# Optimization experiments

Measured on AMD Instinct MI355X. Metric: run time of the kernel, lower is better.

## Reference

```python
import jax, jax.numpy as jnp
from jax import lax
import numpy as np

MSS = 1448.0
MAX_RTT = 0.01
B, S = 2048, 4096


def setup_inputs() -> dict:
    key = jax.random.key(0)
    k1, k2, k3, k4 = jax.random.split(key, 4)
    # packet lengths in [0, 1500) bytes so bursts aggregate past MSS=1448
    x = jax.random.uniform(k1, (B, S), jnp.float32) * 1500.0
    mask = jax.random.uniform(k2, (B, S)) < 0.1
    scale = 0.00094557476340694
    d_exp = 1e-6 + scale * jax.random.exponential(k3, (B, S), jnp.float32)
    delays = jnp.where(mask, jnp.float32(0.21), d_exp)
    # per-burst RTT samples, indexed by the burst-start packet position
    rtts = jax.random.uniform(k4, (B, S), jnp.float32) * MAX_RTT
    return {"x": x, "delays": delays, "rtts": rtts}


def _simulate_row(x, delays, rtts):
    # x, delays, rtts: [S]
    S_ = x.shape[0]

    def step(carry, inp):
        active, new_burst, r = carry
        xj, dj, rj = inp
        # outer-while check only at burst start: stop forever if x[j] <= 0
        active = jnp.where(new_burst, active & (xj > 0), active)
        r = jnp.where(new_burst, rj, r)
        r_next = r - dj  # inner while: RTT -= delays[j]
        burst_end = active & (r_next <= 0)
        start_flag = new_burst & active
        return (active, burst_end, r_next), (active, start_flag)

    init = (jnp.bool_(True), jnp.bool_(True), jnp.float32(0.0))
    _, (consumed, start_flag) = lax.scan(step, init, (x, delays, rtts))

    # per-burst buffered byte count: segment-sum of consumed packet lengths
    burst_id = jnp.clip(jnp.cumsum(start_flag.astype(jnp.int32)) - 1, 0, S_ - 1)
    buf = jax.ops.segment_sum(jnp.where(consumed, x, 0.0), burst_id, num_segments=S_)

    # `while buf > MSS` emits ceil(buf/MSS)-1 full segments, then remainder
    n_full = jnp.maximum(jnp.ceil(buf / MSS).astype(jnp.int32) - 1, 0)
    rem = buf - n_full.astype(x.dtype) * MSS
    has_rem = rem > 0
    count = n_full + has_rem.astype(jnp.int32)
    starts = jnp.cumsum(count) - count  # exclusive cumsum: output offset per burst
    ends = starts + n_full

    # difference-array trick: positions in [starts, ends) get MSS (OOB drops == truncation)
    diff = (jnp.zeros(S_, jnp.int32)
            .at[starts].add(1, mode='drop')
            .at[ends].add(-1, mode='drop'))
    cover = jnp.cumsum(diff) > 0
    out = jnp.where(cover, jnp.float32(MSS), jnp.float32(0.0))

    # remainder goes right after the MSS run of its burst
    rem_pos = jnp.where(has_rem, ends, S_)  # S_ -> dropped
    out = out.at[rem_pos].set(rem, mode='drop')
    return out


def reference(x, delays, rtts):
    out = jax.vmap(_simulate_row)(x, delays, rtts)  # [B, S]
    return out[..., None]  # unsqueeze(-1) -> [B, S, 1]
```

## Files before the change

### kernel.cpp

```cpp
#include <hip/hip_runtime.h>
#include <math.h>


#define S_LEN 4096
#define BLOCK 512
#define PER   8
#define MSSF  1448.0f

#define OFF_A    0
#define OFF_JB   8208
#define OFF_NXT  16416
#define OFF_MENT 24624
#define OFF_WS   25648
#define SMEM_SZ  25680

__global__ __launch_bounds__(BLOCK, 8) void traffic_kernel(
    const float* __restrict__ gx,
    const float* __restrict__ gd,
    const float* __restrict__ gr,
    float* __restrict__ gout)
{
    __shared__ __align__(16) unsigned char smem[SMEM_SZ];
    float*          s_dly  = (float*)(smem + OFF_A);
    unsigned short* s_jA   = (unsigned short*)(smem + OFF_A);
    unsigned short* s_jB   = (unsigned short*)(smem + OFF_JB);
    int*            s_diff = (int*)(smem + OFF_A);
    float*          s_out  = (float*)(smem + OFF_A);
    unsigned short* s_nxt  = (unsigned short*)(smem + OFF_NXT);
    unsigned short* s_ment = (unsigned short*)(smem + OFF_MENT);
    int*            s_ws   = (int*)(smem + OFF_WS);

    const int tid = threadIdx.x;
    const int sb  = tid << 3;
    const size_t rowoff = (size_t)blockIdx.x * S_LEN;
    const float* px = gx + rowoff;
    const float* pd = gd + rowoff;
    const float* pr = gr + rowoff;

    float xreg[PER];
    {
        float4 xa = *(const float4*)(px + sb);
        float4 xb = *(const float4*)(px + sb + 4);
        xreg[0]=xa.x; xreg[1]=xa.y; xreg[2]=xa.z; xreg[3]=xa.w;
        xreg[4]=xb.x; xreg[5]=xb.y; xreg[6]=xb.z; xreg[7]=xb.w;
    }
    {
        const float4* pd4 = (const float4*)pd;
        float4* s4 = (float4*)s_dly;
        for (int q = tid; q < S_LEN / 4; q += BLOCK) s4[q] = pd4[q];
        if (tid < 8) s_dly[S_LEN + tid] = 1.0e30f;
    }
    float rt[PER];
#pragma unroll
    for (int i = 0; i < PER; ++i) rt[i] = pr[tid + (i << 9)];
    __syncthreads();

    unsigned surv = 0;
    float rsv[PER];
#pragma unroll
    for (int i = 0; i < PER; ++i) {
        const int p0 = tid + (i << 9);
        const float* dw = s_dly + p0;
        float d0 = dw[0], d1 = dw[1], d2 = dw[2], d3 = dw[3];
        float d4 = dw[4], d5 = dw[5], d6 = dw[6], d7 = dw[7];
        float r1 = rt[i] - d0;
        float r2 = r1 - d1;
        float r3 = r2 - d2;
        float r4 = r3 - d3;
        float r5 = r4 - d4;
        float r6 = r5 - d5;
        float r7 = r6 - d6;
        float r8 = r7 - d7;
        int c = (r1 > 0.0f) + (r2 > 0.0f) + (r3 > 0.0f) + (r4 > 0.0f) +
                (r5 > 0.0f) + (r6 > 0.0f) + (r7 > 0.0f) + (r8 > 0.0f);
        rsv[i] = r8;
        if (c == 8) {
            surv |= 1u << i;
        } else {
            int nx = p0 + c + 1;
            if (nx > S_LEN) nx = S_LEN;
            s_nxt[p0] = (unsigned short)nx;
        }
    }

    while (surv) {
        int i = __ffs(surv) - 1;
        surv &= surv - 1;
        float rr = rsv[0];
#pragma unroll
        for (int ii = 1; ii < PER; ++ii) rr = (i == ii) ? rsv[ii] : rr;
        int p0 = tid + (i << 9);
        int j = p0 + 8;
        int nx;
        while (true) {
            float e0 = s_dly[j],     e1 = s_dly[j + 1];
            float e2 = s_dly[j + 2], e3 = s_dly[j + 3];
            float e4 = s_dly[j + 4], e5 = s_dly[j + 5];
            float e6 = s_dly[j + 6], e7 = s_dly[j + 7];
            float q1 = rr - e0;
            float q2 = q1 - e1;
            float q3 = q2 - e2;
            float q4 = q3 - e3;
            float q5 = q4 - e4;
            float q6 = q5 - e5;
            float q7 = q6 - e6;
            float q8 = q7 - e7;
            int c2 = (q1 > 0.0f) + (q2 > 0.0f) + (q3 > 0.0f) + (q4 > 0.0f) +
                     (q5 > 0.0f) + (q6 > 0.0f) + (q7 > 0.0f) + (q8 > 0.0f);
            if (c2 < 8) { nx = j + c2 + 1; break; }
            j += 8;
            rr = q8;
        }
        if (nx > S_LEN) nx = S_LEN;
        s_nxt[p0] = (unsigned short)nx;
    }
    __syncthreads();

    int nx8[PER];
    unsigned long long rel = 0x8ull << 32;
    {
        uint4 ld = *(const uint4*)&s_nxt[sb];
        nx8[0] = ld.x & 0xFFFF; nx8[1] = ld.x >> 16;
        nx8[2] = ld.y & 0xFFFF; nx8[3] = ld.y >> 16;
        nx8[4] = ld.z & 0xFFFF; nx8[5] = ld.z >> 16;
        nx8[6] = ld.w & 0xFFFF; nx8[7] = ld.w >> 16;
#pragma unroll
        for (int i = 0; i < PER; ++i)
            if (!(xreg[i] > 0.0f)) nx8[i] = S_LEN;
        int ee[PER];
#pragma unroll
        for (int i = PER - 1; i >= 0; --i) {
            int v = nx8[i];
            int e = v;
#pragma unroll
            for (int j2 = i + 1; j2 < PER; ++j2)
                if (v == sb + j2) e = ee[j2];
            ee[i] = e;
        }
        uint4 pk;
        pk.x = (unsigned)ee[0] | ((unsigned)ee[1] << 16);
        pk.y = (unsigned)ee[2] | ((unsigned)ee[3] << 16);
        pk.z = (unsigned)ee[4] | ((unsigned)ee[5] << 16);
        pk.w = (unsigned)ee[6] | ((unsigned)ee[7] << 16);
        *(uint4*)&s_jA[sb] = pk;
#pragma unroll
        for (int i = 0; i < PER; ++i) {
            int r = nx8[i] - sb; if (r > 8) r = 8;
            rel |= (unsigned long long)r << (i << 2);
        }
    }
    if (tid == 0) { s_jA[4096] = (unsigned short)4096; s_jB[4096] = (unsigned short)4096; }
    s_ment[tid] = (tid == 0) ? (unsigned short)1 : (unsigned short)0;
    __syncthreads();

    {
        unsigned short* ja = s_jA;
        unsigned short* jb = s_jB;
        int own[PER];
#pragma unroll
        for (int i = 0; i < PER; ++i) own[i] = (int)ja[tid + (i << 9)];
        for (int k = 0; k < 9; ++k) {
            int ent = (int)s_ment[tid];
            int q = -1;
            if (ent) {
                int e = (int)ja[ent - 1];
                if (e < S_LEN) q = e;
            }
            if (k < 8) {
                int nv[PER];
#pragma unroll
                for (int i = 0; i < PER; ++i) nv[i] = (int)ja[own[i]];
                if (q >= 0) s_ment[q >> 3] = (unsigned short)(q + 1);
#pragma unroll
                for (int i = 0; i < PER; ++i) jb[tid + (i << 9)] = (unsigned short)nv[i];
#pragma unroll
                for (int i = 0; i < PER; ++i) own[i] = nv[i];
            } else {
                if (q >= 0) s_ment[q >> 3] = (unsigned short)(q + 1);
            }
            __syncthreads();
            unsigned short* t = ja; ja = jb; jb = t;
        }
    }

    unsigned lm = 0;
    {
        int ent = (int)s_ment[tid];
        if (ent) {
            int p = ent - 1 - sb;
#pragma unroll
            for (int s = 0; s < PER; ++s) {
                lm |= (p < 8) ? (1u << p) : 0u;
                p = (int)((rel >> (p << 2)) & 15ull);
            }
        }
    }

    float bsum[PER];
    unsigned use = 0;
    int tsum = 0;
#pragma unroll
    for (int i = 0; i < PER; ++i) {
        float buf = 0.0f;
        int c = 0;
        if ((lm >> i) & 1u) {
            float xp = xreg[i];
            if (xp > 0.0f) {
                use |= 1u << i;
                int e = nx8[i];
                int upper = e - sb;
                float sum = xp;
#pragma unroll
                for (int jj = i + 1; jj < PER; ++jj)
                    sum += (jj < upper) ? xreg[jj] : 0.0f;
                for (int j = sb + PER; j < e; ++j) sum += px[j];
                buf = sum;
                int nf = (int)ceilf(buf / MSSF) - 1; if (nf < 0) nf = 0;
                float rem = buf - (float)nf * MSSF;
                c = nf + (rem > 0.0f ? 1 : 0);
            }
        }
        bsum[i] = buf;
        tsum += c;
    }

    {
        int4* d4 = (int4*)s_diff;
        int4 z; z.x = z.y = z.z = z.w = 0;
        d4[tid] = z;
        d4[tid + 512] = z;
    }
    int texcl;
    {
        int lane = tid & 63, wv = tid >> 6;
        int v = tsum;
        for (int off = 1; off < 64; off <<= 1) {
            int u = __shfl_up(v, off, 64);
            if (lane >= off) v += u;
        }
        if (lane == 63) s_ws[wv] = v;
        __syncthreads();
        int woff = 0;
        for (int w = 0; w < wv; ++w) woff += s_ws[w];
        texcl = woff + v - tsum;
    }

    {
        int o = texcl;
#pragma unroll
        for (int i = 0; i < PER; ++i) {
            if ((use >> i) & 1u) {
                float buf = bsum[i];
                int nf = (int)ceilf(buf / MSSF) - 1; if (nf < 0) nf = 0;
                float rem = buf - (float)nf * MSSF;
                if (nf > 0) {
                    if (o < S_LEN) atomicAdd(&s_diff[o], 1);
                    int e2 = o + nf;
                    if (e2 < S_LEN) atomicAdd(&s_diff[e2], -1);
                }
                o += nf + (rem > 0.0f ? 1 : 0);
            }
        }
    }
    __syncthreads();

    {
        int4 a = *(int4*)&s_diff[sb];
        int4 b = *(int4*)&s_diff[sb + 4];
        int v0 = a.x,      v1 = v0 + a.y, v2 = v1 + a.z, v3 = v2 + a.w;
        int v4 = v3 + b.x, v5 = v4 + b.y, v6 = v5 + b.z, v7 = v6 + b.w;
        int T = v7;
        int lane = tid & 63, wv = tid >> 6;
        int sc = T;
        for (int off = 1; off < 64; off <<= 1) {
            int u = __shfl_up(sc, off, 64);
            if (lane >= off) sc += u;
        }
        if (lane == 63) s_ws[wv] = sc;
        __syncthreads();
        int basev = 0;
        for (int w = 0; w < wv; ++w) basev += s_ws[w];
        basev += sc - T;
        float4 fa, fb;
        fa.x = (basev + v0 > 0) ? MSSF : 0.0f;
        fa.y = (basev + v1 > 0) ? MSSF : 0.0f;
        fa.z = (basev + v2 > 0) ? MSSF : 0.0f;
        fa.w = (basev + v3 > 0) ? MSSF : 0.0f;
        fb.x = (basev + v4 > 0) ? MSSF : 0.0f;
        fb.y = (basev + v5 > 0) ? MSSF : 0.0f;
        fb.z = (basev + v6 > 0) ? MSSF : 0.0f;
        fb.w = (basev + v7 > 0) ? MSSF : 0.0f;
        *(float4*)&s_out[sb]     = fa;
        *(float4*)&s_out[sb + 4] = fb;
    }
    __syncthreads();

    {
        int o = texcl;
#pragma unroll
        for (int i = 0; i < PER; ++i) {
            if ((use >> i) & 1u) {
                float buf = bsum[i];
                int nf = (int)ceilf(buf / MSSF) - 1; if (nf < 0) nf = 0;
                float rem = buf - (float)nf * MSSF;
                int rp = o + nf;
                if (rem > 0.0f && rp < S_LEN) s_out[rp] = rem;
                o += nf + (rem > 0.0f ? 1 : 0);
            }
        }
    }
    __syncthreads();

    {
        float4* po4 = (float4*)(gout + rowoff);
        const float4* so4 = (const float4*)s_out;
        po4[tid]       = so4[tid];
        po4[tid + 512] = so4[tid + 512];
    }
}

extern "C" void kernel_launch(void* const* d_in, const int* in_sizes, int n_in,
                              void* d_out, int out_size, void* d_ws, size_t ws_size,
                              hipStream_t stream) {
    const float* x      = (const float*)d_in[0];
    const float* delays = (const float*)d_in[1];
    const float* rtts   = (const float*)d_in[2];
    float* out = (float*)d_out;
    int rows = in_sizes[0] / S_LEN;
    traffic_kernel<<<rows, BLOCK, 0, stream>>>(x, delays, rtts, out);
}
```

Baseline: 172.8 us.

## Switch to contiguous per-thread positions and keep burst-next indices in registers

The per-position burst-end scan now gives each thread a contiguous run of 8 positions instead of a strided 512-apart mapping. This lets rtts be loaded as float4 and delays read once as 16 registers, and the s_nxt shared buffer and its extra sync/readback go away, since next indices stay in registers. Pointer-jumping writes become packed uint4 stores, the own[] init reuses computed values, and nf/rem are cached instead of recomputing ceil/div three times. Launch bounds drop from 8 to 6 waves per EU to leave room for the larger register footprint, which may lower occupancy.

```diff
diff --git a/kernel.cpp b/kernel.cpp
--- a/kernel.cpp
+++ b/kernel.cpp
@@ -9,12 +9,11 @@
 
 #define OFF_A    0
 #define OFF_JB   8208
-#define OFF_NXT  16416
-#define OFF_MENT 24624
-#define OFF_WS   25648
-#define SMEM_SZ  25680
-
-__global__ __launch_bounds__(BLOCK, 8) void traffic_kernel(
+#define OFF_MENT 16416
+#define OFF_WS   17440
+#define SMEM_SZ  17472
+
+__global__ __launch_bounds__(BLOCK, 6) void traffic_kernel(
     const float* __restrict__ gx,
     const float* __restrict__ gd,
     const float* __restrict__ gr,
@@ -26,7 +25,6 @@
     unsigned short* s_jB   = (unsigned short*)(smem + OFF_JB);
     int*            s_diff = (int*)(smem + OFF_A);
     float*          s_out  = (float*)(smem + OFF_A);
-    unsigned short* s_nxt  = (unsigned short*)(smem + OFF_NXT);
     unsigned short* s_ment = (unsigned short*)(smem + OFF_MENT);
     int*            s_ws   = (int*)(smem + OFF_WS);
 
@@ -38,11 +36,16 @@
     const float* pr = gr + rowoff;
 
     float xreg[PER];
+    float rt[PER];
     {
         float4 xa = *(const float4*)(px + sb);
         float4 xb = *(const float4*)(px + sb + 4);
         xreg[0]=xa.x; xreg[1]=xa.y; xreg[2]=xa.z; xreg[3]=xa.w;
         xreg[4]=xb.x; xreg[5]=xb.y; xreg[6]=xb.z; xreg[7]=xb.w;
+        float4 ra = *(const float4*)(pr + sb);
+        float4 rb = *(const float4*)(pr + sb + 4);
+        rt[0]=ra.x; rt[1]=ra.y; rt[2]=ra.z; rt[3]=ra.w;
+        rt[4]=rb.x; rt[5]=rb.y; rt[6]=rb.z; rt[7]=rb.w;
     }
     {
         const float4* pd4 = (const float4*)pd;
@@ -50,37 +53,38 @@
         for (int q = tid; q < S_LEN / 4; q += BLOCK) s4[q] = pd4[q];
         if (tid < 8) s_dly[S_LEN + tid] = 1.0e30f;
     }
-    float rt[PER];
-#pragma unroll
-    for (int i = 0; i < PER; ++i) rt[i] = pr[tid + (i << 9)];
-    __syncthreads();
+    __syncthreads();
+
+    float dl[16];
+    {
+        const float4* dv = (const float4*)(s_dly + sb);
+        float4 a0 = dv[0], a1 = dv[1], a2 = dv[2], a3 = dv[3];
+        dl[0]=a0.x;  dl[1]=a0.y;  dl[2]=a0.z;  dl[3]=a0.w;
+        dl[4]=a1.x;  dl[5]=a1.y;  dl[6]=a1.z;  dl[7]=a1.w;
+        dl[8]=a2.x;  dl[9]=a2.y;  dl[10]=a2.z; dl[11]=a2.w;
+        dl[12]=a3.x; dl[13]=a3.y; dl[14]=a3.z; dl[15]=a3.w;
+    }
 
     unsigned surv = 0;
     float rsv[PER];
+    int nx8[PER];
 #pragma unroll
     for (int i = 0; i < PER; ++i) {
-        const int p0 = tid + (i << 9);
-        const float* dw = s_dly + p0;
-        float d0 = dw[0], d1 = dw[1], d2 = dw[2], d3 = dw[3];
-        float d4 = dw[4], d5 = dw[5], d6 = dw[6], d7 = dw[7];
-        float r1 = rt[i] - d0;
-        float r2 = r1 - d1;
-        float r3 = r2 - d2;
-        float r4 = r3 - d3;
-        float r5 = r4 - d4;
-        float r6 = r5 - d5;
-        float r7 = r6 - d6;
-        float r8 = r7 - d7;
+        float r1 = rt[i] - dl[i];
+        float r2 = r1 - dl[i + 1];
+        float r3 = r2 - dl[i + 2];
+        float r4 = r3 - dl[i + 3];
+        float r5 = r4 - dl[i + 4];
+        float r6 = r5 - dl[i + 5];
+        float r7 = r6 - dl[i + 6];
+        float r8 = r7 - dl[i + 7];
         int c = (r1 > 0.0f) + (r2 > 0.0f) + (r3 > 0.0f) + (r4 > 0.0f) +
                 (r5 > 0.0f) + (r6 > 0.0f) + (r7 > 0.0f) + (r8 > 0.0f);
         rsv[i] = r8;
-        if (c == 8) {
-            surv |= 1u << i;
-        } else {
-            int nx = p0 + c + 1;
-            if (nx > S_LEN) nx = S_LEN;
-            s_nxt[p0] = (unsigned short)nx;
-        }
+        int nx = sb + i + c + 1;
+        if (nx > S_LEN) nx = S_LEN;
+        nx8[i] = nx;
+        if (c == 8) surv |= 1u << i;
     }
 
     while (surv) {
@@ -89,8 +93,7 @@
         float rr = rsv[0];
 #pragma unroll
         for (int ii = 1; ii < PER; ++ii) rr = (i == ii) ? rsv[ii] : rr;
-        int p0 = tid + (i << 9);
-        int j = p0 + 8;
+        int j = sb + i + 8;
         int nx;
         while (true) {
             float e0 = s_dly[j],     e1 = s_dly[j + 1];
@@ -112,18 +115,14 @@
             rr = q8;
         }
         if (nx > S_LEN) nx = S_LEN;
-        s_nxt[p0] = (unsigned short)nx;
-    }
-    __syncthreads();
-
-    int nx8[PER];
+#pragma unroll
+        for (int ii = 0; ii < PER; ++ii) nx8[ii] = (ii == i) ? nx : nx8[ii];
+    }
+    __syncthreads();
+
+    int own[PER];
     unsigned long long rel = 0x8ull << 32;
     {
-        uint4 ld = *(const uint4*)&s_nxt[sb];
-        nx8[0] = ld.x & 0xFFFF; nx8[1] = ld.x >> 16;
-        nx8[2] = ld.y & 0xFFFF; nx8[3] = ld.y >> 16;
-        nx8[4] = ld.z & 0xFFFF; nx8[5] = ld.z >> 16;
-        nx8[6] = ld.w & 0xFFFF; nx8[7] = ld.w >> 16;
 #pragma unroll
         for (int i = 0; i < PER; ++i)
             if (!(xreg[i] > 0.0f)) nx8[i] = S_LEN;
@@ -148,6 +147,8 @@
             int r = nx8[i] - sb; if (r > 8) r = 8;
             rel |= (unsigned long long)r << (i << 2);
         }
+#pragma unroll
+        for (int i = 0; i < PER; ++i) own[i] = ee[i];
     }
     if (tid == 0) { s_jA[4096] = (unsigned short)4096; s_jB[4096] = (unsigned short)4096; }
     s_ment[tid] = (tid == 0) ? (unsigned short)1 : (unsigned short)0;
@@ -156,9 +157,6 @@
     {
         unsigned short* ja = s_jA;
         unsigned short* jb = s_jB;
-        int own[PER];
-#pragma unroll
-        for (int i = 0; i < PER; ++i) own[i] = (int)ja[tid + (i << 9)];
         for (int k = 0; k < 9; ++k) {
             int ent = (int)s_ment[tid];
             int q = -1;
@@ -171,8 +169,12 @@
 #pragma unroll
                 for (int i = 0; i < PER; ++i) nv[i] = (int)ja[own[i]];
                 if (q >= 0) s_ment[q >> 3] = (unsigned short)(q + 1);
-#pragma unroll
-                for (int i = 0; i < PER; ++i) jb[tid + (i << 9)] = (unsigned short)nv[i];
+                uint4 pk;
+                pk.x = (unsigned)nv[0] | ((unsigned)nv[1] << 16);
+                pk.y = (unsigned)nv[2] | ((unsigned)nv[3] << 16);
+                pk.z = (unsigned)nv[4] | ((unsigned)nv[5] << 16);
+                pk.w = (unsigned)nv[6] | ((unsigned)nv[7] << 16);
+                *(uint4*)&jb[sb] = pk;
 #pragma unroll
                 for (int i = 0; i < PER; ++i) own[i] = nv[i];
             } else {
@@ -196,13 +198,14 @@
         }
     }
 
-    float bsum[PER];
+    int   nf8[PER];
+    float rem8[PER];
     unsigned use = 0;
     int tsum = 0;
 #pragma unroll
     for (int i = 0; i < PER; ++i) {
-        float buf = 0.0f;
-        int c = 0;
+        int nf = 0;
+        float rem = 0.0f;
         if ((lm >> i) & 1u) {
             float xp = xreg[i];
             if (xp > 0.0f) {
@@ -214,14 +217,13 @@
                 for (int jj = i + 1; jj < PER; ++jj)
                     sum += (jj < upper) ? xreg[jj] : 0.0f;
                 for (int j = sb + PER; j < e; ++j) sum += px[j];
-                buf = sum;
-                int nf = (int)ceilf(buf / MSSF) - 1; if (nf < 0) nf = 0;
-                float rem = buf - (float)nf * MSSF;
-                c = nf + (rem > 0.0f ? 1 : 0);
-            }
-        }
-        bsum[i] = buf;
-        tsum += c;
+                nf = (int)ceilf(sum / MSSF) - 1; if (nf < 0) nf = 0;
+                rem = sum - (float)nf * MSSF;
+                tsum += nf + (rem > 0.0f ? 1 : 0);
+            }
+        }
+        nf8[i] = nf;
+        rem8[i] = rem;
     }
 
     {
@@ -250,15 +252,13 @@
 #pragma unroll
         for (int i = 0; i < PER; ++i) {
             if ((use >> i) & 1u) {
-                float buf = bsum[i];
-                int nf = (int)ceilf(buf / MSSF) - 1; if (nf < 0) nf = 0;
-                float rem = buf - (float)nf * MSSF;
+                int nf = nf8[i];
                 if (nf > 0) {
                     if (o < S_LEN) atomicAdd(&s_diff[o], 1);
                     int e2 = o + nf;
                     if (e2 < S_LEN) atomicAdd(&s_diff[e2], -1);
                 }
-                o += nf + (rem > 0.0f ? 1 : 0);
+                o += nf + (rem8[i] > 0.0f ? 1 : 0);
             }
         }
     }
@@ -300,9 +300,8 @@
 #pragma unroll
         for (int i = 0; i < PER; ++i) {
             if ((use >> i) & 1u) {
-                float buf = bsum[i];
-                int nf = (int)ceilf(buf / MSSF) - 1; if (nf < 0) nf = 0;
-                float rem = buf - (float)nf * MSSF;
+                int nf = nf8[i];
+                float rem = rem8[i];
                 int rp = o + nf;
                 if (rem > 0.0f && rp < S_LEN) s_out[rp] = rem;
                 o += nf + (rem > 0.0f ? 1 : 0);
```

Result: no change. 170.3 us (-1.4%).
